# Optimization experiments

Measured on AMD Instinct MI355X. Metric: run time of the kernel, lower is better.

Reference implementation:

```python
import jax, jax.numpy as jnp
import numpy as np

B, L, D = 2, 2048, 2048
H, G, E = 16, 4, 128       # num_heads, group_num, head dim
KV = H // G                # kv heads = 4
OUT = D                    # output_dim == input_dim for residual


def setup_inputs() -> dict:
    key = jax.random.key(0)
    ks = jax.random.split(key, 12)
    s_in = 1.0 / np.sqrt(D)
    s_o = 1.0 / np.sqrt(H * E)
    return {
        "x": jax.random.normal(ks[0], (B, L, D), jnp.float32),
        "Wq": jax.random.normal(ks[1], (D, H * E), jnp.float32) * s_in,
        "bq": jnp.zeros((H * E,), jnp.float32),
        "Wk": jax.random.normal(ks[2], (D, KV * E), jnp.float32) * s_in,
        "bk": jnp.zeros((KV * E,), jnp.float32),
        "Wv": jax.random.normal(ks[3], (D, KV * E), jnp.float32) * s_in,
        "bv": jnp.zeros((KV * E,), jnp.float32),
        "Wo": jax.random.normal(ks[4], (H * E, OUT), jnp.float32) * s_o,
        "bo": jnp.zeros((OUT,), jnp.float32),
        "gamma": jnp.ones((OUT,), jnp.float32),
        "beta": jnp.zeros((OUT,), jnp.float32),
    }


def reference(x, Wq, bq, Wk, bk, Wv, bv, Wo, bo, gamma, beta):
    b, l, _ = x.shape
    Q = (x @ Wq + bq).reshape(b, l, H, E)            # [B,L,H,E]
    K = (x @ Wk + bk).reshape(b, l, KV, E)           # [B,L,KV,E]
    V = (x @ Wv + bv).reshape(b, l, KV, E)
    # GQA expand: reshape(B,L,1,KV,E).expand(G) -> head h = g*KV + kv (tile kv heads G times)
    K = jnp.broadcast_to(K[:, :, None, :, :], (b, l, G, KV, E)).reshape(b, l, H, E)
    V = jnp.broadcast_to(V[:, :, None, :, :], (b, l, G, KV, E)).reshape(b, l, H, E)
    scores = jnp.einsum('blhe,bmhe->bhlm', Q, K) / np.sqrt(E).astype(np.float32)
    # causal mask: triu(ones, diag=1) * -1e9 added to scores
    mask = jnp.triu(jnp.ones((l, l), jnp.float32), k=1) * (-1e9)
    attn = jax.nn.softmax(scores + mask[None, None, :, :], axis=-1)
    ctx = jnp.einsum('bhlm,bmhe->blhe', attn, V).reshape(b, l, H * E)
    y = jax.nn.gelu(ctx @ Wo + bo, approximate=False)  # nn.GELU default = exact erf
    r = x + y
    mu = jnp.mean(r, axis=-1, keepdims=True)
    var = jnp.var(r, axis=-1, keepdims=True)
    return (r - mu) * jax.lax.rsqrt(var + 1e-5) * gamma + beta
```

## Files before the change

kernel.cpp:

```cpp
#include <hip/hip_runtime.h>
#include <hip/hip_bf16.h>
#include <math.h>

typedef __bf16 bf16_t;
typedef __bf16 bf16x4 __attribute__((ext_vector_type(4)));
typedef __bf16 bf16x8 __attribute__((ext_vector_type(8)));
typedef float  f32x4  __attribute__((ext_vector_type(4)));
typedef float  f32x16 __attribute__((ext_vector_type(16)));

#define MFMA16(a,b,c) __builtin_amdgcn_mfma_f32_16x16x32_bf16((a),(b),(c),0,0,0)
#define MFMA32(a,b,c) __builtin_amdgcn_mfma_f32_32x32x16_bf16((a),(b),(c),0,0,0)

#define B_ 2
#define L_ 2048
#define D_ 2048
#define H_ 16
#define KV_ 4
#define E_ 128
#define M_ (B_*L_)
#define NQKV_ 3072

__device__ __forceinline__ void async_ld16(const bf16_t* g, bf16_t* l) {
    __builtin_amdgcn_global_load_lds((const __attribute__((address_space(1))) void*)g,
                                     (__attribute__((address_space(3))) void*)l, 16, 0, 0);
}

__global__ __launch_bounds__(256) void cast_bias_kernel(const float* __restrict__ src,
                                                        bf16_t* __restrict__ dst,
                                                        const float* __restrict__ bq,
                                                        const float* __restrict__ bk,
                                                        const float* __restrict__ bv,
                                                        float* __restrict__ qbias) {
    int bid = blockIdx.x;
    if (bid < 8192) {
        int i = (bid * 256 + threadIdx.x) * 4;
        float4 v = *(const float4*)(src + i);
        bf16x4 o;
        o.x = (bf16_t)v.x; o.y = (bf16_t)v.y; o.z = (bf16_t)v.z; o.w = (bf16_t)v.w;
        *(bf16x4*)(dst + i) = o;
    } else {
        int i = (bid - 8192) * 256 + threadIdx.x;
        if (i < 2048) qbias[i] = bq[i];
        else if (i < 2560) qbias[i] = bk[i - 2048];
        else if (i < 3072) qbias[i] = bv[i - 2560];
    }
}

__global__ __launch_bounds__(256) void wtrans_kernel(const float* __restrict__ Wq,
                                                     const float* __restrict__ Wk,
                                                     const float* __restrict__ Wv,
                                                     const float* __restrict__ Wo,
                                                     bf16_t* __restrict__ WqkvT,
                                                     bf16_t* __restrict__ WoT) {
    __shared__ float tile[32][33];
    int bx = blockIdx.x;
    const float* W; bf16_t* WT; int N, n0;
    if (bx < 64)      { W = Wq; WT = WqkvT;                  N = 2048; n0 = bx * 32; }
    else if (bx < 80) { W = Wk; WT = WqkvT + 2048 * 2048;    N = 512;  n0 = (bx - 64) * 32; }
    else if (bx < 96) { W = Wv; WT = WqkvT + 2560 * 2048;    N = 512;  n0 = (bx - 80) * 32; }
    else              { W = Wo; WT = WoT;                    N = 2048; n0 = (bx - 96) * 32; }
    int k0 = blockIdx.y * 32;
    int tx = threadIdx.x, ty = threadIdx.y;
    #pragma unroll
    for (int i = 0; i < 32; i += 8)
        tile[ty + i][tx] = W[(size_t)(k0 + ty + i) * N + n0 + tx];
    __syncthreads();
    #pragma unroll
    for (int i = 0; i < 32; i += 8)
        WT[(size_t)(n0 + ty + i) * 2048 + k0 + tx] = (bf16_t)tile[tx][ty + i];
}

template <bool OUT_BF16, bool GELU, bool VSPLIT>
__global__ __launch_bounds__(256) void gemm_kernel(const bf16_t* __restrict__ A,
                                                   const bf16_t* __restrict__ BT,
                                                   const float* __restrict__ bias,
                                                   void* __restrict__ C,
                                                   bf16_t* __restrict__ Vt,
                                                   int M, int N, int K) {
    __shared__ __align__(16) bf16_t sA[128][32];
    __shared__ __align__(16) bf16_t sB[128][32];
    int tid = threadIdx.x;
    int wave = tid >> 6, lane = tid & 63;
    int l16 = lane & 15, quad = lane >> 4;
    int flat = blockIdx.y * gridDim.x + blockIdx.x;
    int cpx = (gridDim.x * gridDim.y) >> 3;
    int swz = (flat & 7) * cpx + (flat >> 3);
    int col0 = (swz % gridDim.x) * 128;
    int row0 = (swz / gridDim.x) * 128;
    int wm = (wave >> 1) * 64;
    int wn = (wave & 1) * 64;

    f32x4 acc[4][4];
    #pragma unroll
    for (int i = 0; i < 4; ++i)
        #pragma unroll
        for (int j = 0; j < 4; ++j)
            acc[i][j] = f32x4{0.f, 0.f, 0.f, 0.f};

    for (int k0 = 0; k0 < K; k0 += 32) {
        #pragma unroll
        for (int c = 0; c < 2; ++c) {
            int lin = (c * 256 + tid) * 8;
            int r = lin >> 5, col = lin & 31;
            async_ld16(&A[(size_t)(row0 + r) * K + k0 + col], &sA[r][col]);
            async_ld16(&BT[(size_t)(col0 + r) * K + k0 + col], &sB[r][col]);
        }
        __syncthreads();
        bf16x8 af[4], bf[4];
        #pragma unroll
        for (int mt = 0; mt < 4; ++mt) af[mt] = *(const bf16x8*)&sA[wm + mt * 16 + l16][quad * 8];
        #pragma unroll
        for (int nt = 0; nt < 4; ++nt) bf[nt] = *(const bf16x8*)&sB[wn + nt * 16 + l16][quad * 8];
        #pragma unroll
        for (int mt = 0; mt < 4; ++mt)
            #pragma unroll
            for (int nt = 0; nt < 4; ++nt)
                acc[mt][nt] = MFMA16(af[mt], bf[nt], acc[mt][nt]);
        __syncthreads();
    }

    #pragma unroll
    for (int mt = 0; mt < 4; ++mt) {
        #pragma unroll
        for (int nt = 0; nt < 4; ++nt) {
            int gcol = col0 + wn + nt * 16 + l16;
            float bv = bias[gcol];
            float vv[4];
            #pragma unroll
            for (int r = 0; r < 4; ++r) {
                float v = acc[mt][nt][r] + bv;
                if (GELU) v = 0.5f * v * (1.f + erff(v * 0.70710678118654752f));
                vv[r] = v;
            }
            int grow0 = row0 + wm + mt * 16 + quad * 4;
            if (VSPLIT && gcol >= 2560) {
                int b = grow0 >> 11, l = grow0 & 2047;
                bf16x4 ov;
                #pragma unroll
                for (int r = 0; r < 4; ++r) ov[r] = (bf16_t)vv[r];
                *(bf16x4*)&Vt[((size_t)(b * 512) + (gcol - 2560)) * L_ + l] = ov;
            } else {
                #pragma unroll
                for (int r = 0; r < 4; ++r) {
                    if (OUT_BF16) ((bf16_t*)C)[(size_t)(grow0 + r) * N + gcol] = (bf16_t)vv[r];
                    else          ((float*)C)[(size_t)(grow0 + r) * N + gcol] = vv[r];
                }
            }
        }
    }
}

__global__ __launch_bounds__(128, 2) void attn_kernel(const bf16_t* __restrict__ QKV,
                                                      const bf16_t* __restrict__ Vt,
                                                      bf16_t* __restrict__ Ctx) {
    __shared__ __align__(16) bf16_t sK[2][64][128];

    const int tid = threadIdx.x;
    const int wave = tid >> 6, lane = tid & 63;
    const int l31 = lane & 31, half = lane >> 5;

    const int idx = blockIdx.x;
    const int rr = idx >> 5;
    const int bh = idx & 31;
    const int u = (rr < 8) ? 31 - rr : (rr < 16) ? rr - 8 : (rr < 24) ? 39 - rr : rr - 16;
    const int h = bh & 15, b = bh >> 4;
    const int kv = h & 3;

    const bf16_t* Kbase = QKV + (size_t)b * L_ * NQKV_ + 2048 + kv * 128;
    const bf16_t* Vbase = Vt + (size_t)(b * 4 + kv) * 128 * L_;
    const float SC = 0.12754995f;

    const int qrow = u * 64 + wave * 32 + l31;

    bf16x8 qf[8];
    const bf16_t* Qrow = QKV + (size_t)(b * L_ + qrow) * NQKV_ + h * 128 + half * 8;
    #pragma unroll
    for (int et = 0; et < 8; ++et) qf[et] = *(const bf16x8*)&Qrow[et * 16];

    f32x16 acc[4];
    #pragma unroll
    for (int em = 0; em < 4; ++em)
        #pragma unroll
        for (int j = 0; j < 16; ++j) acc[em][j] = 0.f;
    float l_i = 0.f;

    #define STAGE_K(KT, BUF)                                                          \
        {                                                                             \
            int kk = (KT) * 64;                                                       \
            _Pragma("unroll")                                                         \
            for (int rep = 0; rep < 8; ++rep) {                                       \
                int ch = rep * 128 + tid;                                             \
                int rk = ch >> 4;                                                     \
                int sc = (ch & 15) ^ (rk & 15);                                       \
                async_ld16(&Kbase[(size_t)(kk + rk) * NQKV_ + sc * 8],                \
                           ((bf16_t*)sK[BUF]) + (size_t)ch * 8);                      \
            }                                                                         \
        }

    STAGE_K(0, 0);
    __syncthreads();

    for (int kt = 0; kt <= u; ++kt) {
        const int bufi = kt & 1;
        if (kt < u) STAGE_K(kt + 1, bufi ^ 1);

        bf16x8 vr[16];
        #pragma unroll
        for (int kc = 0; kc < 4; ++kc)
            #pragma unroll
            for (int em = 0; em < 4; ++em)
                vr[kc * 4 + em] = *(const bf16x8*)&Vbase[(size_t)(em * 32 + l31) * L_ +
                                                         kt * 64 + (kc * 2 + half) * 8];

        f32x16 s[2];
        #pragma unroll
        for (int mt = 0; mt < 2; ++mt)
            #pragma unroll
            for (int j = 0; j < 16; ++j) s[mt][j] = 0.f;
        __builtin_amdgcn_s_setprio(1);
        #pragma unroll
        for (int mt = 0; mt < 2; ++mt)
            #pragma unroll
            for (int et = 0; et < 8; ++et) {
                bf16x8 kf = *(const bf16x8*)&sK[bufi][mt * 32 + l31][((et * 2 + half) ^ (l31 & 15)) * 8];
                s[mt] = MFMA32(kf, qf[et], s[mt]);
            }
        __builtin_amdgcn_s_setprio(0);

        if (kt == u) {
            #pragma unroll
            for (int mt = 0; mt < 2; ++mt)
                #pragma unroll
                for (int j = 0; j < 16; ++j) {
                    int kidx = kt * 64 + mt * 32 + (j & 3) + 8 * (j >> 2) + 4 * half;
                    if (kidx > qrow) s[mt][j] = -3.0e38f;
                }
        }

        float rs = 0.f;
        #pragma unroll
        for (int mt = 0; mt < 2; ++mt)
            #pragma unroll
            for (int j = 0; j < 16; ++j) {
                float p = exp2f(s[mt][j] * SC);
                s[mt][j] = p;
                rs += p;
            }
        rs += __shfl_xor(rs, 32, 64);
        l_i += rs;

        bf16x4 pk[2][4];
        #pragma unroll
        for (int mt = 0; mt < 2; ++mt)
            #pragma unroll
            for (int g = 0; g < 4; ++g) {
                bf16x4 tt;
                #pragma unroll
                for (int i = 0; i < 4; ++i) tt[i] = (bf16_t)s[mt][g * 4 + i];
                pk[mt][g] = tt;
            }

        #pragma unroll
        for (int kc = 0; kc < 4; ++kc) {
            const int mts = kc >> 1, g0 = 2 * (kc & 1);
            bf16x4 send = half ? pk[mts][g0] : pk[mts][g0 + 1];
            bf16x4 keep = half ? pk[mts][g0 + 1] : pk[mts][g0];
            union { bf16x4 v; int i[2]; } su, ru;
            su.v = send;
            ru.i[0] = __shfl_xor(su.i[0], 32, 64);
            ru.i[1] = __shfl_xor(su.i[1], 32, 64);
            bf16x4 lo = half ? ru.v : keep;
            bf16x4 hi = half ? keep : ru.v;
            bf16x8 pf = __builtin_shufflevector(lo, hi, 0, 1, 2, 3, 4, 5, 6, 7);
            __builtin_amdgcn_s_setprio(1);
            #pragma unroll
            for (int em = 0; em < 4; ++em)
                acc[em] = MFMA32(vr[kc * 4 + em], pf, acc[em]);
            __builtin_amdgcn_s_setprio(0);
        }

        __syncthreads();
    }

    const float inv = 1.f / l_i;
    bf16_t* Cp = Ctx + (size_t)(b * L_ + qrow) * 2048 + h * 128;
    #pragma unroll
    for (int em = 0; em < 4; ++em)
        #pragma unroll
        for (int g = 0; g < 4; ++g) {
            bf16x4 ov;
            #pragma unroll
            for (int i = 0; i < 4; ++i) ov[i] = (bf16_t)(acc[em][g * 4 + i] * inv);
            *(bf16x4*)&Cp[em * 32 + g * 8 + half * 4] = ov;
        }
}

__global__ __launch_bounds__(256) void ln_kernel(const bf16_t* __restrict__ Y,
                                                 const float* __restrict__ X,
                                                 const float* __restrict__ gamma,
                                                 const float* __restrict__ beta,
                                                 float* __restrict__ out) {
    __shared__ float sr[2048];
    __shared__ float wred[8];
    size_t row = blockIdx.x;
    const bf16_t* y = Y + row * 2048;
    const float* x = X + row * 2048;
    float sum = 0.f, ssq = 0.f;
    #pragma unroll
    for (int c = 0; c < 2; ++c) {
        int i = (c * 256 + threadIdx.x) * 4;
        bf16x4 yv = *(const bf16x4*)(y + i);
        float4 xv = *(const float4*)(x + i);
        float r0 = xv.x + (float)yv[0];
        float r1 = xv.y + (float)yv[1];
        float r2 = xv.z + (float)yv[2];
        float r3 = xv.w + (float)yv[3];
        sr[i] = r0; sr[i + 1] = r1; sr[i + 2] = r2; sr[i + 3] = r3;
        sum += r0 + r1 + r2 + r3;
        ssq += r0 * r0 + r1 * r1 + r2 * r2 + r3 * r3;
    }
    #pragma unroll
    for (int off = 32; off > 0; off >>= 1) {
        sum += __shfl_xor(sum, off, 64);
        ssq += __shfl_xor(ssq, off, 64);
    }
    int wv = threadIdx.x >> 6;
    if ((threadIdx.x & 63) == 0) { wred[wv] = sum; wred[wv + 4] = ssq; }
    __syncthreads();
    sum = wred[0] + wred[1] + wred[2] + wred[3];
    ssq = wred[4] + wred[5] + wred[6] + wred[7];
    float mu = sum * (1.f / 2048.f);
    float var = ssq * (1.f / 2048.f) - mu * mu;
    float rstd = rsqrtf(var + 1e-5f);
    #pragma unroll
    for (int c = 0; c < 2; ++c) {
        int i = (c * 256 + threadIdx.x) * 4;
        float4 gv = *(const float4*)(gamma + i);
        float4 bv = *(const float4*)(beta + i);
        float4 o;
        o.x = (sr[i]     - mu) * rstd * gv.x + bv.x;
        o.y = (sr[i + 1] - mu) * rstd * gv.y + bv.y;
        o.z = (sr[i + 2] - mu) * rstd * gv.z + bv.z;
        o.w = (sr[i + 3] - mu) * rstd * gv.w + bv.w;
        *(float4*)(out + row * 2048 + i) = o;
    }
}

extern "C" void kernel_launch(void* const* d_in, const int* in_sizes, int n_in,
                              void* d_out, int out_size, void* d_ws, size_t ws_size,
                              hipStream_t stream) {
    const float* x     = (const float*)d_in[0];
    const float* Wq    = (const float*)d_in[1];
    const float* bq    = (const float*)d_in[2];
    const float* Wk    = (const float*)d_in[3];
    const float* bk    = (const float*)d_in[4];
    const float* Wv    = (const float*)d_in[5];
    const float* bv    = (const float*)d_in[6];
    const float* Wo    = (const float*)d_in[7];
    const float* bo    = (const float*)d_in[8];
    const float* gamma = (const float*)d_in[9];
    const float* beta  = (const float*)d_in[10];
    float* out = (float*)d_out;

    char* ws = (char*)d_ws;
    size_t off = 0;
    bf16_t* xb    = (bf16_t*)(ws + off); off += 16777216;
    bf16_t* WqkvT = (bf16_t*)(ws + off); off += 12582912;
    bf16_t* WoT   = (bf16_t*)(ws + off); off += 8388608;
    float*  qbias = (float*)(ws + off);  off += 12288;
    bf16_t* QKV   = (bf16_t*)(ws + off); off += 25165824;
    bf16_t* Vt    = (bf16_t*)(ws + off); off += 4194304;
    bf16_t* Cb    = (bf16_t*)(ws + off); off += 16777216;
    bf16_t* Yb    = (bf16_t*)(ws + off); off += 16777216;

    cast_bias_kernel<<<8204, 256, 0, stream>>>(x, xb, bq, bk, bv, qbias);
    wtrans_kernel<<<dim3(160, 64), dim3(32, 8), 0, stream>>>(Wq, Wk, Wv, Wo, WqkvT, WoT);

    gemm_kernel<true, false, true><<<dim3(24, 32), 256, 0, stream>>>(xb, WqkvT, qbias, QKV, Vt, M_, NQKV_, D_);
    attn_kernel<<<1024, 128, 0, stream>>>(QKV, Vt, Cb);
    gemm_kernel<true, true, false><<<dim3(16, 32), 256, 0, stream>>>(Cb, WoT, bo, Yb, nullptr, M_, D_, 2048);
    ln_kernel<<<M_, 256, 0, stream>>>(Yb, x, gamma, beta, out);
}
```

Before: 352.1 us.

## Replace QKV projection GEMM with 256x256 double-buffered pipelined kernel

Adds a new 512-thread GEMM kernel with 256x256 output tiles, a 64-wide K step, XOR-swizzled LDS layout and double-buffered async global-to-LDS loads. Loads for upcoming K tiles are staggered across four compute phases, with explicit vmcnt waits, barriers and s_setprio around the MFMA blocks. Only the QKV projection uses it. The larger tile raises data reuse and the pipelining hides load latency. In exchange LDS use is much higher (128 KB per block) and the grid shrinks to 192 blocks, which is below one wave of blocks across the CUs and may leave some idle.

```diff
diff --git a/kernel.cpp b/kernel.cpp
--- a/kernel.cpp
+++ b/kernel.cpp
@@ -70,12 +70,143 @@
         WT[(size_t)(n0 + ty + i) * 2048 + k0 + tx] = (bf16_t)tile[tx][ty + i];
 }
 
-template <bool OUT_BF16, bool GELU, bool VSPLIT>
+template <bool VSPLIT>
+__global__ __launch_bounds__(512, 2) void gemm256_kernel(const bf16_t* __restrict__ A,
+                                                         const bf16_t* __restrict__ BT,
+                                                         const float* __restrict__ bias,
+                                                         bf16_t* __restrict__ C,
+                                                         bf16_t* __restrict__ Vt,
+                                                         int M, int N, int K) {
+    __shared__ __align__(16) bf16_t sA[2][256][64];
+    __shared__ __align__(16) bf16_t sB[2][256][64];
+    const int tid = threadIdx.x;
+    const int wave = tid >> 6, lane = tid & 63;
+    const int l16 = lane & 15, quad = lane >> 4;
+    const int wrow = (wave >> 2) * 64;
+    const int wcol = (wave & 3) * 32;
+
+    int flat = blockIdx.y * gridDim.x + blockIdx.x;
+    int cpx = (gridDim.x * gridDim.y) >> 3;
+    int swz = (flat & 7) * cpx + (flat >> 3);
+    int col0 = (swz % gridDim.x) * 256;
+    int row0 = (swz / gridDim.x) * 256;
+
+    const int NT = K >> 6;
+
+    #define STAGE_HALF(KT, BUF, ISB, HALF)                                            \
+        {                                                                             \
+            const bf16_t* Gp = (ISB) ? BT : A;                                        \
+            int brow_ = ((ISB) ? col0 : row0) + (HALF) * 128;                         \
+            bf16_t* Lp = (ISB) ? &sB[BUF][(HALF) * 128][0] : &sA[BUF][(HALF) * 128][0];\
+            _Pragma("unroll")                                                         \
+            for (int rep_ = 0; rep_ < 2; ++rep_) {                                    \
+                int ch_ = rep_ * 512 + tid;                                           \
+                int rr_ = ch_ >> 3, cp_ = ch_ & 7;                                    \
+                int cl_ = cp_ ^ (rr_ & 7);                                            \
+                async_ld16(&Gp[(size_t)(brow_ + rr_) * K + (KT) * 64 + cl_ * 8],      \
+                           Lp + ch_ * 8);                                             \
+            }                                                                         \
+        }
+
+    f32x4 acc[4][4][2];
+    #pragma unroll
+    for (int ph = 0; ph < 4; ++ph)
+        #pragma unroll
+        for (int fm = 0; fm < 4; ++fm)
+            #pragma unroll
+            for (int fn = 0; fn < 2; ++fn)
+                acc[ph][fm][fn] = f32x4{0.f, 0.f, 0.f, 0.f};
+
+    STAGE_HALF(0, 0, 0, 0); STAGE_HALF(0, 0, 1, 0); STAGE_HALF(0, 0, 0, 1); STAGE_HALF(0, 0, 1, 1);
+    STAGE_HALF(1, 1, 0, 0); STAGE_HALF(1, 1, 1, 0); STAGE_HALF(1, 1, 0, 1); STAGE_HALF(1, 1, 1, 1);
+    asm volatile("s_waitcnt vmcnt(8)" ::: "memory");
+    __builtin_amdgcn_s_barrier();
+    __builtin_amdgcn_sched_barrier(0);
+
+    for (int t = 0; t < NT; ++t) {
+        const int bufi = t & 1;
+        #pragma unroll
+        for (int ph = 0; ph < 4; ++ph) {
+            const int qm = ph >> 1, qn = ph & 1;
+            bf16x8 af[4][2], bf[2][2];
+            #pragma unroll
+            for (int fm = 0; fm < 4; ++fm) {
+                int r = qm * 128 + wrow + fm * 16 + l16;
+                #pragma unroll
+                for (int kk = 0; kk < 2; ++kk) {
+                    int cc = (kk * 4 + quad) ^ (r & 7);
+                    af[fm][kk] = *(const bf16x8*)&sA[bufi][r][cc * 8];
+                }
+            }
+            #pragma unroll
+            for (int fn = 0; fn < 2; ++fn) {
+                int r = qn * 128 + wcol + fn * 16 + l16;
+                #pragma unroll
+                for (int kk = 0; kk < 2; ++kk) {
+                    int cc = (kk * 4 + quad) ^ (r & 7);
+                    bf[fn][kk] = *(const bf16x8*)&sB[bufi][r][cc * 8];
+                }
+            }
+            if (ph == 0)      { if (t >= 1 && t + 1 < NT) STAGE_HALF(t + 1, (t + 1) & 1, 1, 1); }
+            else if (ph == 1) { if (t + 2 < NT) STAGE_HALF(t + 2, bufi, 0, 0); }
+            else if (ph == 2) { if (t + 2 < NT) STAGE_HALF(t + 2, bufi, 1, 0); }
+            else              { if (t + 2 < NT) STAGE_HALF(t + 2, bufi, 0, 1); }
+
+            __builtin_amdgcn_s_barrier();
+            __builtin_amdgcn_sched_barrier(0);
+            __builtin_amdgcn_s_setprio(1);
+            #pragma unroll
+            for (int fm = 0; fm < 4; ++fm)
+                #pragma unroll
+                for (int fn = 0; fn < 2; ++fn)
+                    #pragma unroll
+                    for (int kk = 0; kk < 2; ++kk)
+                        acc[ph][fm][fn] = MFMA16(af[fm][kk], bf[fn][kk], acc[ph][fm][fn]);
+            __builtin_amdgcn_s_setprio(0);
+            if (ph == 3) {
+                if (t < NT - 2) { asm volatile("s_waitcnt vmcnt(6)" ::: "memory"); }
+                else            { asm volatile("s_waitcnt vmcnt(0)" ::: "memory"); }
+            }
+            __builtin_amdgcn_s_barrier();
+            __builtin_amdgcn_sched_barrier(0);
+        }
+    }
+
+    #pragma unroll
+    for (int ph = 0; ph < 4; ++ph) {
+        const int qm = ph >> 1, qn = ph & 1;
+        #pragma unroll
+        for (int fm = 0; fm < 4; ++fm) {
+            #pragma unroll
+            for (int fn = 0; fn < 2; ++fn) {
+                int gcol = col0 + qn * 128 + wcol + fn * 16 + l16;
+                float bv = bias[gcol];
+                int grow0 = row0 + qm * 128 + wrow + fm * 16 + quad * 4;
+                float vv[4];
+                #pragma unroll
+                for (int r = 0; r < 4; ++r) vv[r] = acc[ph][fm][fn][r] + bv;
+                if (VSPLIT && gcol >= 2560) {
+                    int b = grow0 >> 11, l = grow0 & 2047;
+                    bf16x4 ov;
+                    #pragma unroll
+                    for (int r = 0; r < 4; ++r) ov[r] = (bf16_t)vv[r];
+                    *(bf16x4*)&Vt[((size_t)(b * 512) + (gcol - 2560)) * L_ + l] = ov;
+                } else {
+                    #pragma unroll
+                    for (int r = 0; r < 4; ++r)
+                        C[(size_t)(grow0 + r) * N + gcol] = (bf16_t)vv[r];
+                }
+            }
+        }
+    }
+    #undef STAGE_HALF
+}
+
+template <bool OUT_BF16, bool GELU>
 __global__ __launch_bounds__(256) void gemm_kernel(const bf16_t* __restrict__ A,
                                                    const bf16_t* __restrict__ BT,
                                                    const float* __restrict__ bias,
                                                    void* __restrict__ C,
-                                                   bf16_t* __restrict__ Vt,
                                                    int M, int N, int K) {
     __shared__ __align__(16) bf16_t sA[128][32];
     __shared__ __align__(16) bf16_t sB[128][32];
@@ -125,26 +256,13 @@
         for (int nt = 0; nt < 4; ++nt) {
             int gcol = col0 + wn + nt * 16 + l16;
             float bv = bias[gcol];
-            float vv[4];
             #pragma unroll
             for (int r = 0; r < 4; ++r) {
+                int grow = row0 + wm + mt * 16 + quad * 4 + r;
                 float v = acc[mt][nt][r] + bv;
                 if (GELU) v = 0.5f * v * (1.f + erff(v * 0.70710678118654752f));
-                vv[r] = v;
-            }
-            int grow0 = row0 + wm + mt * 16 + quad * 4;
-            if (VSPLIT && gcol >= 2560) {
-                int b = grow0 >> 11, l = grow0 & 2047;
-                bf16x4 ov;
-                #pragma unroll
-                for (int r = 0; r < 4; ++r) ov[r] = (bf16_t)vv[r];
-                *(bf16x4*)&Vt[((size_t)(b * 512) + (gcol - 2560)) * L_ + l] = ov;
-            } else {
-                #pragma unroll
-                for (int r = 0; r < 4; ++r) {
-                    if (OUT_BF16) ((bf16_t*)C)[(size_t)(grow0 + r) * N + gcol] = (bf16_t)vv[r];
-                    else          ((float*)C)[(size_t)(grow0 + r) * N + gcol] = vv[r];
-                }
+                if (OUT_BF16) ((bf16_t*)C)[(size_t)grow * N + gcol] = (bf16_t)v;
+                else          ((float*)C)[(size_t)grow * N + gcol] = v;
             }
         }
     }
@@ -376,8 +494,8 @@
     cast_bias_kernel<<<8204, 256, 0, stream>>>(x, xb, bq, bk, bv, qbias);
     wtrans_kernel<<<dim3(160, 64), dim3(32, 8), 0, stream>>>(Wq, Wk, Wv, Wo, WqkvT, WoT);
 
-    gemm_kernel<true, false, true><<<dim3(24, 32), 256, 0, stream>>>(xb, WqkvT, qbias, QKV, Vt, M_, NQKV_, D_);
+    gemm256_kernel<true><<<dim3(12, 16), 512, 0, stream>>>(xb, WqkvT, qbias, QKV, Vt, M_, NQKV_, D_);
     attn_kernel<<<1024, 128, 0, stream>>>(QKV, Vt, Cb);
-    gemm_kernel<true, true, false><<<dim3(16, 32), 256, 0, stream>>>(Cb, WoT, bo, Yb, nullptr, M_, D_, 2048);
+    gemm_kernel<true, true><<<dim3(16, 32), 256, 0, stream>>>(Cb, WoT, bo, Yb, M_, D_, 2048);
     ln_kernel<<<M_, 256, 0, stream>>>(Yb, x, gamma, beta, out);
 }
```

Measured after the change: 361.7 us. 2.7% more time.

## Double GEMM K-tile to 64 with XOR-swizzled LDS layout

Applied to the files above, without the earlier changes.

The GEMM kernel now stages a 64-wide K slice per iteration instead of 32, halving the number of barrier pairs per K loop. It also applies an XOR swizzle on 16-byte chunks when writing and reading LDS to reduce bank conflicts on the fragment loads. The unused fp32 output template path is dropped. LDS use per block doubles to 32 KB, which may lower occupancy somewhat, and the loop still has no double buffering.

```diff
diff --git a/kernel.cpp b/kernel.cpp
--- a/kernel.cpp
+++ b/kernel.cpp
@@ -70,15 +70,15 @@
         WT[(size_t)(n0 + ty + i) * 2048 + k0 + tx] = (bf16_t)tile[tx][ty + i];
 }
 
-template <bool OUT_BF16, bool GELU, bool VSPLIT>
+template <bool GELU, bool VSPLIT>
 __global__ __launch_bounds__(256) void gemm_kernel(const bf16_t* __restrict__ A,
                                                    const bf16_t* __restrict__ BT,
                                                    const float* __restrict__ bias,
-                                                   void* __restrict__ C,
+                                                   bf16_t* __restrict__ C,
                                                    bf16_t* __restrict__ Vt,
                                                    int M, int N, int K) {
-    __shared__ __align__(16) bf16_t sA[128][32];
-    __shared__ __align__(16) bf16_t sB[128][32];
+    __shared__ __align__(16) bf16_t sA[128][64];
+    __shared__ __align__(16) bf16_t sB[128][64];
     int tid = threadIdx.x;
     int wave = tid >> 6, lane = tid & 63;
     int l16 = lane & 15, quad = lane >> 4;
@@ -97,25 +97,35 @@
         for (int j = 0; j < 4; ++j)
             acc[i][j] = f32x4{0.f, 0.f, 0.f, 0.f};
 
-    for (int k0 = 0; k0 < K; k0 += 32) {
-        #pragma unroll
-        for (int c = 0; c < 2; ++c) {
-            int lin = (c * 256 + tid) * 8;
-            int r = lin >> 5, col = lin & 31;
-            async_ld16(&A[(size_t)(row0 + r) * K + k0 + col], &sA[r][col]);
-            async_ld16(&BT[(size_t)(col0 + r) * K + k0 + col], &sB[r][col]);
+    for (int k0 = 0; k0 < K; k0 += 64) {
+        #pragma unroll
+        for (int c = 0; c < 4; ++c) {
+            int ch = c * 256 + tid;
+            int r = ch >> 3, cp = ch & 7;
+            int cl = cp ^ (r & 7);
+            async_ld16(&A[(size_t)(row0 + r) * K + k0 + cl * 8], &sA[r][cp * 8]);
+            async_ld16(&BT[(size_t)(col0 + r) * K + k0 + cl * 8], &sB[r][cp * 8]);
         }
         __syncthreads();
-        bf16x8 af[4], bf[4];
-        #pragma unroll
-        for (int mt = 0; mt < 4; ++mt) af[mt] = *(const bf16x8*)&sA[wm + mt * 16 + l16][quad * 8];
-        #pragma unroll
-        for (int nt = 0; nt < 4; ++nt) bf[nt] = *(const bf16x8*)&sB[wn + nt * 16 + l16][quad * 8];
-        #pragma unroll
-        for (int mt = 0; mt < 4; ++mt)
-            #pragma unroll
-            for (int nt = 0; nt < 4; ++nt)
-                acc[mt][nt] = MFMA16(af[mt], bf[nt], acc[mt][nt]);
+        #pragma unroll
+        for (int kk = 0; kk < 2; ++kk) {
+            bf16x8 af[4], bf[4];
+            #pragma unroll
+            for (int mt = 0; mt < 4; ++mt) {
+                int r = wm + mt * 16 + l16;
+                af[mt] = *(const bf16x8*)&sA[r][((kk * 4 + quad) ^ (r & 7)) * 8];
+            }
+            #pragma unroll
+            for (int nt = 0; nt < 4; ++nt) {
+                int r = wn + nt * 16 + l16;
+                bf[nt] = *(const bf16x8*)&sB[r][((kk * 4 + quad) ^ (r & 7)) * 8];
+            }
+            #pragma unroll
+            for (int mt = 0; mt < 4; ++mt)
+                #pragma unroll
+                for (int nt = 0; nt < 4; ++nt)
+                    acc[mt][nt] = MFMA16(af[mt], bf[nt], acc[mt][nt]);
+        }
         __syncthreads();
     }
 
@@ -141,10 +151,8 @@
                 *(bf16x4*)&Vt[((size_t)(b * 512) + (gcol - 2560)) * L_ + l] = ov;
             } else {
                 #pragma unroll
-                for (int r = 0; r < 4; ++r) {
-                    if (OUT_BF16) ((bf16_t*)C)[(size_t)(grow0 + r) * N + gcol] = (bf16_t)vv[r];
-                    else          ((float*)C)[(size_t)(grow0 + r) * N + gcol] = vv[r];
-                }
+                for (int r = 0; r < 4; ++r)
+                    C[(size_t)(grow0 + r) * N + gcol] = (bf16_t)vv[r];
             }
         }
     }
@@ -376,8 +384,8 @@
     cast_bias_kernel<<<8204, 256, 0, stream>>>(x, xb, bq, bk, bv, qbias);
     wtrans_kernel<<<dim3(160, 64), dim3(32, 8), 0, stream>>>(Wq, Wk, Wv, Wo, WqkvT, WoT);
 
-    gemm_kernel<true, false, true><<<dim3(24, 32), 256, 0, stream>>>(xb, WqkvT, qbias, QKV, Vt, M_, NQKV_, D_);
+    gemm_kernel<false, true><<<dim3(24, 32), 256, 0, stream>>>(xb, WqkvT, qbias, QKV, Vt, M_, NQKV_, D_);
     attn_kernel<<<1024, 128, 0, stream>>>(QKV, Vt, Cb);
-    gemm_kernel<true, true, false><<<dim3(16, 32), 256, 0, stream>>>(Cb, WoT, bo, Yb, nullptr, M_, D_, 2048);
+    gemm_kernel<true, false><<<dim3(16, 32), 256, 0, stream>>>(Cb, WoT, bo, Yb, nullptr, M_, D_, 2048);
     ln_kernel<<<M_, 256, 0, stream>>>(Yb, x, gamma, beta, out);
 }
```

New measurement: 339.0 us. 3.7% less time.
